# Kernel tuning notes

Hardware: AMD Instinct MI355X
Metric: run time of the kernel (lower is better)

Reference implementation:

```python
import jax, jax.numpy as jnp
import numpy as np

HEADS = 8
HEAD_DIM = 32
INNER = HEADS * HEAD_DIM  # 256
DIM = 256
WS = 8            # window_size
DISP = WS // 2    # displacement for shifted windows
SCALE = HEAD_DIM ** -0.5
NEG_INF = float('-inf')


def _rel_indices(ws):
    # [ws^2, ws^2, 2] relative (dy, dx) offsets shifted to be >= 0
    idx = np.array([[x, y] for x in range(ws) for y in range(ws)])
    return idx[None, :, :] - idx[:, None, :] + ws - 1

REL = _rel_indices(WS)


def _create_mask(ws, disp, upper_lower, left_right):
    m = np.zeros((ws * ws, ws * ws), dtype=np.float32)
    if upper_lower:
        m[-disp * ws:, :-disp * ws] = NEG_INF
        m[:-disp * ws, -disp * ws:] = NEG_INF
    if left_right:
        m = m.reshape(ws, ws, ws, ws)
        m[:, -disp:, :, :-disp] = NEG_INF
        m[:, :-disp, :, -disp:] = NEG_INF
        m = m.reshape(ws * ws, ws * ws)
    return m

UL_MASK = _create_mask(WS, DISP, True, False)
LR_MASK = _create_mask(WS, DISP, False, True)


def setup_inputs() -> dict:
    key = jax.random.key(0)
    k1, k2, k3, k4 = jax.random.split(key, 4)
    x = jax.random.normal(k1, (8, 128, 128, DIM), dtype=jnp.float32)
    w_qkv = jax.random.normal(k2, (DIM, 3 * INNER), dtype=jnp.float32) * 0.02
    pos_embedding = jax.random.normal(k3, (2 * WS - 1, 2 * WS - 1), dtype=jnp.float32)
    w_out = jax.random.normal(k4, (INNER, DIM), dtype=jnp.float32) * 0.02
    b_out = jnp.zeros((DIM,), dtype=jnp.float32)
    return {"x": x, "w_qkv": w_qkv, "pos_embedding": pos_embedding,
            "w_out": w_out, "b_out": b_out}


def reference(x, w_qkv, pos_embedding, w_out, b_out):
    b, H, W, _ = x.shape
    nwh, nww = H // WS, W // WS
    nw = nwh * nww

    # cyclic shift (shifted=True)
    xs = jnp.roll(x, (-DISP, -DISP), axis=(1, 2))

    qkv = xs @ w_qkv  # [b, H, W, 3*INNER]
    q, k, v = jnp.split(qkv, 3, axis=-1)

    def to_windows(t):
        # [b,H,W,INNER] -> [b, heads, nw, ws*ws, head_dim]
        t = t.reshape(b, nwh, WS, nww, WS, HEADS, HEAD_DIM)
        return t.transpose(0, 5, 1, 3, 2, 4, 6).reshape(b, HEADS, nw, WS * WS, HEAD_DIM)

    q, k, v = to_windows(q), to_windows(k), to_windows(v)

    dots = jnp.einsum('bhwid,bhwjd->bhwij', q, k) * SCALE

    # relative position bias gather: [ws^2, ws^2]
    bias = pos_embedding[REL[..., 0], REL[..., 1]]
    dots = dots + bias

    # shifted-window mask (static per grid): [nw, ws^2, ws^2]
    mask = np.zeros((nw, WS * WS, WS * WS), dtype=np.float32)
    mask[-nww:] += UL_MASK
    mask[nww - 1::nww] += LR_MASK
    dots = dots + jnp.asarray(mask)

    attn = jax.nn.softmax(dots, axis=-1)
    out = jnp.einsum('bhwij,bhwjd->bhwid', attn, v)

    # windows -> [b, H, W, INNER]
    out = out.reshape(b, HEADS, nwh, nww, WS, WS, HEAD_DIM)
    out = out.transpose(0, 2, 4, 3, 5, 1, 6).reshape(b, H, W, INNER)

    out = out @ w_out + b_out
    out = jnp.roll(out, (DISP, DISP), axis=(1, 2))  # cyclic back shift
    return out
```

## Files before the change

### kernel.cpp

```cpp
#include <hip/hip_runtime.h>
#include <hip/hip_bf16.h>


typedef __attribute__((ext_vector_type(8)))  short bf16x8;
typedef __attribute__((ext_vector_type(16))) float f32x16;

#define MFMA32(a, b, c) __builtin_amdgcn_mfma_f32_32x32x16_bf16((a), (b), (c), 0, 0, 0)

#define QK_SCALE 0.17677669529663687f
#define LOG2E    1.44269504088896340f

__device__ __forceinline__ uint32_t pack2(float lo, float hi) {
  float2 f2; f2.x = lo; f2.y = hi;
  __hip_bfloat162 h2 = __float22bfloat162_rn(f2);
  union { __hip_bfloat162 h; uint32_t u; } cv;
  cv.h = h2;
  return cv.u;
}

__device__ __forceinline__ bf16x8 frag_from_u4(uint32_t a, uint32_t b,
                                               uint32_t c, uint32_t d) {
  union { uint32_t u[4]; bf16x8 v; } r;
  r.u[0] = a; r.u[1] = b; r.u[2] = c; r.u[3] = d;
  return r.v;
}

__device__ __forceinline__ bf16x8 makefrag(const f32x16& a, int kt, int hf) {
  const int b0 = kt * 8;
  uint32_t q0 = pack2(a[b0 + 0], a[b0 + 1]);
  uint32_t q1 = pack2(a[b0 + 2], a[b0 + 3]);
  uint32_t q2 = pack2(a[b0 + 4], a[b0 + 5]);
  uint32_t q3 = pack2(a[b0 + 6], a[b0 + 7]);
  uint32_t x0 = (uint32_t)__shfl_xor((int)q0, 32, 64);
  uint32_t x1 = (uint32_t)__shfl_xor((int)q1, 32, 64);
  uint32_t x2 = (uint32_t)__shfl_xor((int)q2, 32, 64);
  uint32_t x3 = (uint32_t)__shfl_xor((int)q3, 32, 64);
  uint32_t d0 = hf ? x2 : q0;
  uint32_t d1 = hf ? x3 : q1;
  uint32_t d2 = hf ? q2 : x0;
  uint32_t d3 = hf ? q3 : x1;
  return frag_from_u4(d0, d1, d2, d3);
}

__global__ void prep_weights(const float* __restrict__ wqkv,
                             const float* __restrict__ wout,
                             const float* __restrict__ pos,
                             ushort* __restrict__ Wpack,
                             ushort* __restrict__ WoPack,
                             float* __restrict__ Bpack) {
  int id = blockIdx.x * 256 + threadIdx.x;
  if (id < 196608) {
    int sec = id >> 16;
    int j = id & 65535;
    int h = j >> 13, kt = (j >> 9) & 15, lane = (j >> 3) & 63, i = j & 7;
    int n = h * 32 + (lane & 31);
    int k = kt * 16 + (lane >> 5) * 8 + i;
    float v = wqkv[k * 768 + sec * 256 + n];
    if (sec == 0) v *= QK_SCALE;
    Wpack[id] = __bfloat16_as_ushort(__float2bfloat16(v));
  } else if (id < 262144) {
    int j = id - 196608;
    int h = j >> 13, kt = (j >> 9) & 15, lane = (j >> 3) & 63, i = j & 7;
    int n = h * 32 + (lane & 31);
    int k = kt * 16 + (lane >> 5) * 8 + i;
    WoPack[j] = __bfloat16_as_ushort(__float2bfloat16(wout[k * 256 + n]));
  } else if (id < 278528) {
    int j = id - 262144;
    int type = j >> 12;
    int r12 = j & 4095;
    int ai = r12 >> 11, bi = (r12 >> 10) & 1, rb = (r12 >> 8) & 3;
    int lane = (r12 >> 2) & 63, jj = r12 & 3;
    int n = jj + 8 * rb + 4 * (lane >> 5) + 32 * ai;
    int m = (lane & 31) + 32 * bi;
    float v = pos[((n >> 3) - (m >> 3) + 7) * 15 + ((n & 7) - (m & 7) + 7)];
    bool ul = (m >= 32) != (n >= 32);
    bool lr = ((m & 7) >= 4) != ((n & 7) >= 4);
    if (((type & 2) && ul) || ((type & 1) && lr)) v = -1e30f;
    Bpack[j] = v;
  }
}

__global__ __launch_bounds__(512, 2) void swin_attn(
    const float* __restrict__ x, const float* __restrict__ bout,
    const ushort* __restrict__ Wpack, const ushort* __restrict__ WoPack,
    const float* __restrict__ Bpack, float* __restrict__ out) {
  __shared__ uint4 lds[32 * 64];
  uint4*  ldsX = lds;
  ushort* ldsO = (ushort*)lds;

  const int bid = blockIdx.x;
  const int b  = bid >> 8;
  const int wy = (bid >> 4) & 15;
  const int wx = bid & 15;
  const int t    = threadIdx.x;
  const int lane = t & 63;
  const int h    = t >> 6;
  const int l31  = lane & 31;
  const int hf   = lane >> 5;

  f32x16 zf;
  #pragma unroll
  for (int i = 0; i < 16; ++i) zf[i] = 0.0f;

  {
    int tok = t >> 3, kc = t & 7;
    int ty = tok >> 3, tx = tok & 7;
    int yy = (wy * 8 + ty + 4) & 127;
    int xx = (wx * 8 + tx + 4) & 127;
    const float* xr = x + (((b * 128 + yy) * 128 + xx) << 8) + kc * 32;
    #pragma unroll
    for (int g = 0; g < 4; ++g) {
      float4 a = *(const float4*)(xr + g * 8);
      float4 c = *(const float4*)(xr + g * 8 + 4);
      uint4 w;
      w.x = pack2(a.x, a.y); w.y = pack2(a.z, a.w);
      w.z = pack2(c.x, c.y); w.w = pack2(c.z, c.w);
      int kg = kc * 4 + g;
      ldsX[(kg * 64 + tok) ^ kc] = w;
    }
  }
  __syncthreads();

  const ushort* wqp = Wpack + h * 8192;
  const ushort* wkp = wqp + 65536;
  const ushort* wvp = wkp + 65536;

  bf16x8 fQ[2][2];
  {
    f32x16 a0 = zf, a1 = zf;
    #pragma unroll 4
    for (int kt = 0; kt < 16; ++kt) {
      int kg = 2 * kt + hf;
      uint4 ux0 = ldsX[(kg * 64 + l31) ^ (kg >> 2)];
      uint4 ux1 = ldsX[(kg * 64 + 32 + l31) ^ (kg >> 2)];
      bf16x8 xf0 = frag_from_u4(ux0.x, ux0.y, ux0.z, ux0.w);
      bf16x8 xf1 = frag_from_u4(ux1.x, ux1.y, ux1.z, ux1.w);
      bf16x8 fw = *(const bf16x8*)(wqp + kt * 512 + lane * 8);
      a0 = MFMA32(fw, xf0, a0);  a1 = MFMA32(fw, xf1, a1);
    }
    #pragma unroll
    for (int kt = 0; kt < 2; ++kt) {
      fQ[0][kt] = makefrag(a0, kt, hf);
      fQ[1][kt] = makefrag(a1, kt, hf);
    }
  }

  bf16x8 fK[2][2];
  {
    f32x16 a0 = zf, a1 = zf;
    #pragma unroll 4
    for (int kt = 0; kt < 16; ++kt) {
      int kg = 2 * kt + hf;
      uint4 ux0 = ldsX[(kg * 64 + l31) ^ (kg >> 2)];
      uint4 ux1 = ldsX[(kg * 64 + 32 + l31) ^ (kg >> 2)];
      bf16x8 xf0 = frag_from_u4(ux0.x, ux0.y, ux0.z, ux0.w);
      bf16x8 xf1 = frag_from_u4(ux1.x, ux1.y, ux1.z, ux1.w);
      bf16x8 fw = *(const bf16x8*)(wkp + kt * 512 + lane * 8);
      a0 = MFMA32(fw, xf0, a0);  a1 = MFMA32(fw, xf1, a1);
    }
    #pragma unroll
    for (int kt = 0; kt < 2; ++kt) {
      fK[0][kt] = makefrag(a0, kt, hf);
      fK[1][kt] = makefrag(a1, kt, hf);
    }
  }

  const float* Bp = Bpack + ((((wy == 15) ? 2 : 0) | ((wx == 15) ? 1 : 0)) << 12);
  bf16x8 pf[2][4];
  float ri[2];
  #pragma unroll
  for (int bi = 0; bi < 2; ++bi) {
    f32x16 s0, s1;
    #pragma unroll
    for (int rb = 0; rb < 4; ++rb) {
      float4 f0 = *(const float4*)(Bp + ((bi * 4 + rb) * 64 + lane) * 4);
      float4 f1 = *(const float4*)(Bp + (((2 + bi) * 4 + rb) * 64 + lane) * 4);
      s0[rb * 4 + 0] = f0.x; s0[rb * 4 + 1] = f0.y;
      s0[rb * 4 + 2] = f0.z; s0[rb * 4 + 3] = f0.w;
      s1[rb * 4 + 0] = f1.x; s1[rb * 4 + 1] = f1.y;
      s1[rb * 4 + 2] = f1.z; s1[rb * 4 + 3] = f1.w;
    }
    #pragma unroll
    for (int kt = 0; kt < 2; ++kt) {
      s0 = MFMA32(fK[0][kt], fQ[bi][kt], s0);
      s1 = MFMA32(fK[1][kt], fQ[bi][kt], s1);
    }
    float mx = -3e38f;
    #pragma unroll
    for (int r = 0; r < 16; ++r) mx = fmaxf(mx, fmaxf(s0[r], s1[r]));
    mx = fmaxf(mx, __shfl_xor(mx, 32, 64));
    float sum = 0.0f;
    #pragma unroll
    for (int r = 0; r < 16; ++r) {
      float p0 = exp2f((s0[r] - mx) * LOG2E);
      float p1 = exp2f((s1[r] - mx) * LOG2E);
      s0[r] = p0; s1[r] = p1;
      sum += p0 + p1;
    }
    sum += __shfl_xor(sum, 32, 64);
    ri[bi] = 1.0f / sum;
    #pragma unroll
    for (int kt = 0; kt < 2; ++kt) {
      pf[bi][kt]     = makefrag(s0, kt, hf);
      pf[bi][2 + kt] = makefrag(s1, kt, hf);
    }
  }

  bf16x8 fV[2][2];
  {
    f32x16 a0 = zf, a1 = zf;
    #pragma unroll 4
    for (int kt = 0; kt < 16; ++kt) {
      int kg = 2 * kt + hf;
      uint4 ux0 = ldsX[(kg * 64 + l31) ^ (kg >> 2)];
      uint4 ux1 = ldsX[(kg * 64 + 32 + l31) ^ (kg >> 2)];
      bf16x8 xf0 = frag_from_u4(ux0.x, ux0.y, ux0.z, ux0.w);
      bf16x8 xf1 = frag_from_u4(ux1.x, ux1.y, ux1.z, ux1.w);
      bf16x8 fw = *(const bf16x8*)(wvp + kt * 512 + lane * 8);
      a0 = MFMA32(xf0, fw, a0);  a1 = MFMA32(xf1, fw, a1);
    }
    #pragma unroll
    for (int kt = 0; kt < 2; ++kt) {
      fV[0][kt] = makefrag(a0, kt, hf);
      fV[1][kt] = makefrag(a1, kt, hf);
    }
  }

  f32x16 ot[2];
  ot[0] = zf; ot[1] = zf;
  #pragma unroll
  for (int jt = 0; jt < 4; ++jt) {
    bf16x8 aV = fV[jt >> 1][jt & 1];
    ot[0] = MFMA32(aV, pf[0][jt], ot[0]);
    ot[1] = MFMA32(aV, pf[1][jt], ot[1]);
  }
  #pragma unroll
  for (int bi = 0; bi < 2; ++bi)
    #pragma unroll
    for (int r = 0; r < 16; ++r) ot[bi][r] *= ri[bi];

  __syncthreads();

  {
    #pragma unroll
    for (int bi = 0; bi < 2; ++bi) {
      int tok = bi * 32 + l31;
      #pragma unroll
      for (int g = 0; g < 4; ++g) {
        int kg = h * 4 + g;
        uint2 wv2;
        wv2.x = pack2(ot[bi][4 * g + 0], ot[bi][4 * g + 1]);
        wv2.y = pack2(ot[bi][4 * g + 2], ot[bi][4 * g + 3]);
        *(uint2*)&ldsO[(kg * 64 + tok) * 8 + 4 * hf] = wv2;
      }
    }
  }
  __syncthreads();

  const ushort* wop = WoPack + h * 8192;
  f32x16 u[2];
  u[0] = zf; u[1] = zf;
  #pragma unroll 4
  for (int kt = 0; kt < 16; ++kt) {
    int kg = 2 * kt + hf;
    bf16x8 wa = *(const bf16x8*)(wop + kt * 512 + lane * 8);
    bf16x8 b0 = *(const bf16x8*)&ldsO[(kg * 64 + l31) * 8];
    bf16x8 b1 = *(const bf16x8*)&ldsO[(kg * 64 + 32 + l31) * 8];
    u[0] = MFMA32(wa, b0, u[0]);
    u[1] = MFMA32(wa, b1, u[1]);
  }

  #pragma unroll
  for (int tt = 0; tt < 2; ++tt) {
    int tok = 32 * tt + l31;
    int ty = tok >> 3, tx = tok & 7;
    int yy = (wy * 8 + ty + 4) & 127;
    int xx = (wx * 8 + tx + 4) & 127;
    float* ob = out + (((b * 128 + yy) * 128 + xx) << 8);
    #pragma unroll
    for (int g = 0; g < 4; ++g) {
      int c0 = h * 32 + 8 * g + 4 * hf;
      float4 bo = *(const float4*)(bout + c0);
      float4 v;
      v.x = (tt ? u[1][4 * g + 0] : u[0][4 * g + 0]) + bo.x;
      v.y = (tt ? u[1][4 * g + 1] : u[0][4 * g + 1]) + bo.y;
      v.z = (tt ? u[1][4 * g + 2] : u[0][4 * g + 2]) + bo.z;
      v.w = (tt ? u[1][4 * g + 3] : u[0][4 * g + 3]) + bo.w;
      *(float4*)(ob + c0) = v;
    }
  }
}

extern "C" void kernel_launch(void* const* d_in, const int* in_sizes, int n_in,
                              void* d_out, int out_size, void* d_ws, size_t ws_size,
                              hipStream_t stream) {
  const float* x    = (const float*)d_in[0];
  const float* wqkv = (const float*)d_in[1];
  const float* pos  = (const float*)d_in[2];
  const float* wout = (const float*)d_in[3];
  const float* bout = (const float*)d_in[4];

  ushort* Wpack  = (ushort*)d_ws;
  ushort* WoPack = Wpack + 196608;
  float*  Bpack  = (float*)((char*)d_ws + 524288);

  prep_weights<<<1088, 256, 0, stream>>>(wqkv, wout, pos, Wpack, WoPack, Bpack);
  swin_attn<<<2048, 512, 0, stream>>>(x, bout, Wpack, WoPack, Bpack, (float*)d_out);
}
```

Before: 140.3 us.

## Process two adjacent windows per block to reuse weight fragments

Each block now computes two neighbouring shifted windows instead of one. Every weight fragment fetched from global memory feeds four MFMAs instead of two, and the grid is halved. This targets redundant weight loads per window. In exchange, LDS use doubles and register pressure rises, which may reduce occupancy or cause spills under the existing launch bounds.

Result: slower. 158.7 us (+13.1%).

```diff
diff --git a/kernel.cpp b/kernel.cpp
--- a/kernel.cpp
+++ b/kernel.cpp
@@ -84,14 +84,14 @@
     const float* __restrict__ x, const float* __restrict__ bout,
     const ushort* __restrict__ Wpack, const ushort* __restrict__ WoPack,
     const float* __restrict__ Bpack, float* __restrict__ out) {
-  __shared__ uint4 lds[32 * 64];
+  __shared__ uint4 lds[2 * 32 * 64];
   uint4*  ldsX = lds;
   ushort* ldsO = (ushort*)lds;
 
   const int bid = blockIdx.x;
-  const int b  = bid >> 8;
-  const int wy = (bid >> 4) & 15;
-  const int wx = bid & 15;
+  const int b   = bid >> 7;
+  const int wy  = (bid >> 3) & 15;
+  const int wxp = bid & 7;
   const int t    = threadIdx.x;
   const int lane = t & 63;
   const int h    = t >> 6;
@@ -106,17 +106,21 @@
     int tok = t >> 3, kc = t & 7;
     int ty = tok >> 3, tx = tok & 7;
     int yy = (wy * 8 + ty + 4) & 127;
-    int xx = (wx * 8 + tx + 4) & 127;
-    const float* xr = x + (((b * 128 + yy) * 128 + xx) << 8) + kc * 32;
-    #pragma unroll
-    for (int g = 0; g < 4; ++g) {
-      float4 a = *(const float4*)(xr + g * 8);
-      float4 c = *(const float4*)(xr + g * 8 + 4);
-      uint4 w;
-      w.x = pack2(a.x, a.y); w.y = pack2(a.z, a.w);
-      w.z = pack2(c.x, c.y); w.w = pack2(c.z, c.w);
-      int kg = kc * 4 + g;
-      ldsX[(kg * 64 + tok) ^ kc] = w;
+    #pragma unroll
+    for (int w = 0; w < 2; ++w) {
+      int wx = wxp * 2 + w;
+      int xx = (wx * 8 + tx + 4) & 127;
+      const float* xr = x + (((b * 128 + yy) * 128 + xx) << 8) + kc * 32;
+      #pragma unroll
+      for (int g = 0; g < 4; ++g) {
+        float4 a = *(const float4*)(xr + g * 8);
+        float4 c = *(const float4*)(xr + g * 8 + 4);
+        uint4 wv;
+        wv.x = pack2(a.x, a.y); wv.y = pack2(a.z, a.w);
+        wv.z = pack2(c.x, c.y); wv.w = pack2(c.z, c.w);
+        int kg = kc * 4 + g;
+        ldsX[w * 2048 + ((kg * 64 + tok) ^ kc)] = wv;
+      }
     }
   }
   __syncthreads();
@@ -125,123 +129,149 @@
   const ushort* wkp = wqp + 65536;
   const ushort* wvp = wkp + 65536;
 
-  bf16x8 fQ[2][2];
+  bf16x8 fQ0[2][2], fQ1[2][2];
   {
-    f32x16 a0 = zf, a1 = zf;
-    #pragma unroll 4
+    f32x16 a00 = zf, a01 = zf, a10 = zf, a11 = zf;
+    #pragma unroll 2
     for (int kt = 0; kt < 16; ++kt) {
       int kg = 2 * kt + hf;
-      uint4 ux0 = ldsX[(kg * 64 + l31) ^ (kg >> 2)];
-      uint4 ux1 = ldsX[(kg * 64 + 32 + l31) ^ (kg >> 2)];
-      bf16x8 xf0 = frag_from_u4(ux0.x, ux0.y, ux0.z, ux0.w);
-      bf16x8 xf1 = frag_from_u4(ux1.x, ux1.y, ux1.z, ux1.w);
+      int s0i = (kg * 64 + l31) ^ (kg >> 2);
+      int s1i = (kg * 64 + 32 + l31) ^ (kg >> 2);
+      uint4 u00 = ldsX[s0i],        u01 = ldsX[s1i];
+      uint4 u10 = ldsX[2048 + s0i], u11 = ldsX[2048 + s1i];
       bf16x8 fw = *(const bf16x8*)(wqp + kt * 512 + lane * 8);
-      a0 = MFMA32(fw, xf0, a0);  a1 = MFMA32(fw, xf1, a1);
+      a00 = MFMA32(fw, frag_from_u4(u00.x, u00.y, u00.z, u00.w), a00);
+      a01 = MFMA32(fw, frag_from_u4(u01.x, u01.y, u01.z, u01.w), a01);
+      a10 = MFMA32(fw, frag_from_u4(u10.x, u10.y, u10.z, u10.w), a10);
+      a11 = MFMA32(fw, frag_from_u4(u11.x, u11.y, u11.z, u11.w), a11);
     }
     #pragma unroll
     for (int kt = 0; kt < 2; ++kt) {
-      fQ[0][kt] = makefrag(a0, kt, hf);
-      fQ[1][kt] = makefrag(a1, kt, hf);
-    }
-  }
-
-  bf16x8 fK[2][2];
+      fQ0[0][kt] = makefrag(a00, kt, hf);
+      fQ0[1][kt] = makefrag(a01, kt, hf);
+      fQ1[0][kt] = makefrag(a10, kt, hf);
+      fQ1[1][kt] = makefrag(a11, kt, hf);
+    }
+  }
+
+  bf16x8 fK0[2][2], fK1[2][2];
   {
-    f32x16 a0 = zf, a1 = zf;
-    #pragma unroll 4
+    f32x16 a00 = zf, a01 = zf, a10 = zf, a11 = zf;
+    #pragma unroll 2
     for (int kt = 0; kt < 16; ++kt) {
       int kg = 2 * kt + hf;
-      uint4 ux0 = ldsX[(kg * 64 + l31) ^ (kg >> 2)];
-      uint4 ux1 = ldsX[(kg * 64 + 32 + l31) ^ (kg >> 2)];
-      bf16x8 xf0 = frag_from_u4(ux0.x, ux0.y, ux0.z, ux0.w);
-      bf16x8 xf1 = frag_from_u4(ux1.x, ux1.y, ux1.z, ux1.w);
+      int s0i = (kg * 64 + l31) ^ (kg >> 2);
+      int s1i = (kg * 64 + 32 + l31) ^ (kg >> 2);
+      uint4 u00 = ldsX[s0i],        u01 = ldsX[s1i];
+      uint4 u10 = ldsX[2048 + s0i], u11 = ldsX[2048 + s1i];
       bf16x8 fw = *(const bf16x8*)(wkp + kt * 512 + lane * 8);
-      a0 = MFMA32(fw, xf0, a0);  a1 = MFMA32(fw, xf1, a1);
+      a00 = MFMA32(fw, frag_from_u4(u00.x, u00.y, u00.z, u00.w), a00);
+      a01 = MFMA32(fw, frag_from_u4(u01.x, u01.y, u01.z, u01.w), a01);
+      a10 = MFMA32(fw, frag_from_u4(u10.x, u10.y, u10.z, u10.w), a10);
+      a11 = MFMA32(fw, frag_from_u4(u11.x, u11.y, u11.z, u11.w), a11);
     }
     #pragma unroll
     for (int kt = 0; kt < 2; ++kt) {
-      fK[0][kt] = makefrag(a0, kt, hf);
-      fK[1][kt] = makefrag(a1, kt, hf);
-    }
-  }
-
-  const float* Bp = Bpack + ((((wy == 15) ? 2 : 0) | ((wx == 15) ? 1 : 0)) << 12);
-  bf16x8 pf[2][4];
-  float ri[2];
+      fK0[0][kt] = makefrag(a00, kt, hf);
+      fK0[1][kt] = makefrag(a01, kt, hf);
+      fK1[0][kt] = makefrag(a10, kt, hf);
+      fK1[1][kt] = makefrag(a11, kt, hf);
+    }
+  }
+
+  bf16x8 pf0[2][4], pf1[2][4];
+  float ri0[2], ri1[2];
+  const int tybase = (wy == 15) ? 2 : 0;
   #pragma unroll
-  for (int bi = 0; bi < 2; ++bi) {
-    f32x16 s0, s1;
-    #pragma unroll
-    for (int rb = 0; rb < 4; ++rb) {
-      float4 f0 = *(const float4*)(Bp + ((bi * 4 + rb) * 64 + lane) * 4);
-      float4 f1 = *(const float4*)(Bp + (((2 + bi) * 4 + rb) * 64 + lane) * 4);
-      s0[rb * 4 + 0] = f0.x; s0[rb * 4 + 1] = f0.y;
-      s0[rb * 4 + 2] = f0.z; s0[rb * 4 + 3] = f0.w;
-      s1[rb * 4 + 0] = f1.x; s1[rb * 4 + 1] = f1.y;
-      s1[rb * 4 + 2] = f1.z; s1[rb * 4 + 3] = f1.w;
-    }
-    #pragma unroll
-    for (int kt = 0; kt < 2; ++kt) {
-      s0 = MFMA32(fK[0][kt], fQ[bi][kt], s0);
-      s1 = MFMA32(fK[1][kt], fQ[bi][kt], s1);
-    }
-    float mx = -3e38f;
-    #pragma unroll
-    for (int r = 0; r < 16; ++r) mx = fmaxf(mx, fmaxf(s0[r], s1[r]));
-    mx = fmaxf(mx, __shfl_xor(mx, 32, 64));
-    float sum = 0.0f;
-    #pragma unroll
-    for (int r = 0; r < 16; ++r) {
-      float p0 = exp2f((s0[r] - mx) * LOG2E);
-      float p1 = exp2f((s1[r] - mx) * LOG2E);
-      s0[r] = p0; s1[r] = p1;
-      sum += p0 + p1;
-    }
-    sum += __shfl_xor(sum, 32, 64);
-    ri[bi] = 1.0f / sum;
-    #pragma unroll
-    for (int kt = 0; kt < 2; ++kt) {
-      pf[bi][kt]     = makefrag(s0, kt, hf);
-      pf[bi][2 + kt] = makefrag(s1, kt, hf);
-    }
-  }
-
-  bf16x8 fV[2][2];
-  {
-    f32x16 a0 = zf, a1 = zf;
-    #pragma unroll 4
-    for (int kt = 0; kt < 16; ++kt) {
-      int kg = 2 * kt + hf;
-      uint4 ux0 = ldsX[(kg * 64 + l31) ^ (kg >> 2)];
-      uint4 ux1 = ldsX[(kg * 64 + 32 + l31) ^ (kg >> 2)];
-      bf16x8 xf0 = frag_from_u4(ux0.x, ux0.y, ux0.z, ux0.w);
-      bf16x8 xf1 = frag_from_u4(ux1.x, ux1.y, ux1.z, ux1.w);
-      bf16x8 fw = *(const bf16x8*)(wvp + kt * 512 + lane * 8);
-      a0 = MFMA32(xf0, fw, a0);  a1 = MFMA32(xf1, fw, a1);
-    }
-    #pragma unroll
-    for (int kt = 0; kt < 2; ++kt) {
-      fV[0][kt] = makefrag(a0, kt, hf);
-      fV[1][kt] = makefrag(a1, kt, hf);
-    }
-  }
-
-  f32x16 ot[2];
-  ot[0] = zf; ot[1] = zf;
+  for (int w = 0; w < 2; ++w) {
+    int wx = wxp * 2 + w;
+    const float* Bp = Bpack + ((tybase | ((wx == 15) ? 1 : 0)) << 12);
+    #pragma unroll
+    for (int bi = 0; bi < 2; ++bi) {
+      f32x16 s0, s1;
+      #pragma unroll
+      for (int rb = 0; rb < 4; ++rb) {
+        float4 f0 = *(const float4*)(Bp + ((bi * 4 + rb) * 64 + lane) * 4);
+        float4 f1 = *(const float4*)(Bp + (((2 + bi) * 4 + rb) * 64 + lane) * 4);
+        s0[rb * 4 + 0] = f0.x; s0[rb * 4 + 1] = f0.y;
+        s0[rb * 4 + 2] = f0.z; s0[rb * 4 + 3] = f0.w;
+        s1[rb * 4 + 0] = f1.x; s1[rb * 4 + 1] = f1.y;
+        s1[rb * 4 + 2] = f1.z; s1[rb * 4 + 3] = f1.w;
+      }
+      #pragma unroll
+      for (int kt = 0; kt < 2; ++kt) {
+        s0 = MFMA32(w ? fK1[0][kt] : fK0[0][kt],
+                    w ? fQ1[bi][kt] : fQ0[bi][kt], s0);
+        s1 = MFMA32(w ? fK1[1][kt] : fK0[1][kt],
+                    w ? fQ1[bi][kt] : fQ0[bi][kt], s1);
+      }
+      float mx = -3e38f;
+      #pragma unroll
+      for (int r = 0; r < 16; ++r) mx = fmaxf(mx, fmaxf(s0[r], s1[r]));
+      mx = fmaxf(mx, __shfl_xor(mx, 32, 64));
+      float sum = 0.0f;
+      #pragma unroll
+      for (int r = 0; r < 16; ++r) {
+        float p0 = exp2f((s0[r] - mx) * LOG2E);
+        float p1 = exp2f((s1[r] - mx) * LOG2E);
+        s0[r] = p0; s1[r] = p1;
+        sum += p0 + p1;
+      }
+      sum += __shfl_xor(sum, 32, 64);
+      float rv = 1.0f / sum;
+      if (w) ri1[bi] = rv; else ri0[bi] = rv;
+      #pragma unroll
+      for (int kt = 0; kt < 2; ++kt) {
+        if (w) {
+          pf1[bi][kt]     = makefrag(s0, kt, hf);
+          pf1[bi][2 + kt] = makefrag(s1, kt, hf);
+        } else {
+          pf0[bi][kt]     = makefrag(s0, kt, hf);
+          pf0[bi][2 + kt] = makefrag(s1, kt, hf);
+        }
+      }
+    }
+  }
+
   #pragma unroll
-  for (int jt = 0; jt < 4; ++jt) {
-    bf16x8 aV = fV[jt >> 1][jt & 1];
-    ot[0] = MFMA32(aV, pf[0][jt], ot[0]);
-    ot[1] = MFMA32(aV, pf[1][jt], ot[1]);
-  }
-  #pragma unroll
-  for (int bi = 0; bi < 2; ++bi)
-    #pragma unroll
-    for (int r = 0; r < 16; ++r) ot[bi][r] *= ri[bi];
-
-  __syncthreads();
-
-  {
+  for (int w = 0; w < 2; ++w) {
+    bf16x8 fV[2][2];
+    {
+      f32x16 a0 = zf, a1 = zf;
+      #pragma unroll 2
+      for (int kt = 0; kt < 16; ++kt) {
+        int kg = 2 * kt + hf;
+        int s0i = (kg * 64 + l31) ^ (kg >> 2);
+        int s1i = (kg * 64 + 32 + l31) ^ (kg >> 2);
+        uint4 ux0 = ldsX[w * 2048 + s0i];
+        uint4 ux1 = ldsX[w * 2048 + s1i];
+        bf16x8 fw = *(const bf16x8*)(wvp + kt * 512 + lane * 8);
+        a0 = MFMA32(frag_from_u4(ux0.x, ux0.y, ux0.z, ux0.w), fw, a0);
+        a1 = MFMA32(frag_from_u4(ux1.x, ux1.y, ux1.z, ux1.w), fw, a1);
+      }
+      #pragma unroll
+      for (int kt = 0; kt < 2; ++kt) {
+        fV[0][kt] = makefrag(a0, kt, hf);
+        fV[1][kt] = makefrag(a1, kt, hf);
+      }
+    }
+    __syncthreads();
+
+    f32x16 ot[2];
+    ot[0] = zf; ot[1] = zf;
+    #pragma unroll
+    for (int jt = 0; jt < 4; ++jt) {
+      bf16x8 aV = fV[jt >> 1][jt & 1];
+      ot[0] = MFMA32(aV, w ? pf1[0][jt] : pf0[0][jt], ot[0]);
+      ot[1] = MFMA32(aV, w ? pf1[1][jt] : pf0[1][jt], ot[1]);
+    }
+    #pragma unroll
+    for (int bi = 0; bi < 2; ++bi) {
+      float rv = w ? ri1[bi] : ri0[bi];
+      #pragma unroll
+      for (int r = 0; r < 16; ++r) ot[bi][r] *= rv;
+    }
+
     #pragma unroll
     for (int bi = 0; bi < 2; ++bi) {
       int tok = bi * 32 + l31;
@@ -251,42 +281,48 @@
         uint2 wv2;
         wv2.x = pack2(ot[bi][4 * g + 0], ot[bi][4 * g + 1]);
         wv2.y = pack2(ot[bi][4 * g + 2], ot[bi][4 * g + 3]);
-        *(uint2*)&ldsO[(kg * 64 + tok) * 8 + 4 * hf] = wv2;
+        *(uint2*)&ldsO[w * 16384 + (kg * 64 + tok) * 8 + 4 * hf] = wv2;
       }
     }
   }
   __syncthreads();
 
   const ushort* wop = WoPack + h * 8192;
-  f32x16 u[2];
-  u[0] = zf; u[1] = zf;
-  #pragma unroll 4
+  f32x16 u00 = zf, u01 = zf, u10 = zf, u11 = zf;
+  #pragma unroll 2
   for (int kt = 0; kt < 16; ++kt) {
     int kg = 2 * kt + hf;
     bf16x8 wa = *(const bf16x8*)(wop + kt * 512 + lane * 8);
-    bf16x8 b0 = *(const bf16x8*)&ldsO[(kg * 64 + l31) * 8];
-    bf16x8 b1 = *(const bf16x8*)&ldsO[(kg * 64 + 32 + l31) * 8];
-    u[0] = MFMA32(wa, b0, u[0]);
-    u[1] = MFMA32(wa, b1, u[1]);
+    bf16x8 b00 = *(const bf16x8*)&ldsO[(kg * 64 + l31) * 8];
+    bf16x8 b01 = *(const bf16x8*)&ldsO[(kg * 64 + 32 + l31) * 8];
+    bf16x8 b10 = *(const bf16x8*)&ldsO[16384 + (kg * 64 + l31) * 8];
+    bf16x8 b11 = *(const bf16x8*)&ldsO[16384 + (kg * 64 + 32 + l31) * 8];
+    u00 = MFMA32(wa, b00, u00);  u01 = MFMA32(wa, b01, u01);
+    u10 = MFMA32(wa, b10, u10);  u11 = MFMA32(wa, b11, u11);
   }
 
   #pragma unroll
-  for (int tt = 0; tt < 2; ++tt) {
-    int tok = 32 * tt + l31;
-    int ty = tok >> 3, tx = tok & 7;
-    int yy = (wy * 8 + ty + 4) & 127;
-    int xx = (wx * 8 + tx + 4) & 127;
-    float* ob = out + (((b * 128 + yy) * 128 + xx) << 8);
-    #pragma unroll
-    for (int g = 0; g < 4; ++g) {
-      int c0 = h * 32 + 8 * g + 4 * hf;
-      float4 bo = *(const float4*)(bout + c0);
-      float4 v;
-      v.x = (tt ? u[1][4 * g + 0] : u[0][4 * g + 0]) + bo.x;
-      v.y = (tt ? u[1][4 * g + 1] : u[0][4 * g + 1]) + bo.y;
-      v.z = (tt ? u[1][4 * g + 2] : u[0][4 * g + 2]) + bo.z;
-      v.w = (tt ? u[1][4 * g + 3] : u[0][4 * g + 3]) + bo.w;
-      *(float4*)(ob + c0) = v;
+  for (int w = 0; w < 2; ++w) {
+    int wx = wxp * 2 + w;
+    #pragma unroll
+    for (int tt = 0; tt < 2; ++tt) {
+      const f32x16& u = w ? (tt ? u11 : u10) : (tt ? u01 : u00);
+      int tok = 32 * tt + l31;
+      int ty = tok >> 3, tx = tok & 7;
+      int yy = (wy * 8 + ty + 4) & 127;
+      int xx = (wx * 8 + tx + 4) & 127;
+      float* ob = out + (((b * 128 + yy) * 128 + xx) << 8);
+      #pragma unroll
+      for (int g = 0; g < 4; ++g) {
+        int c0 = h * 32 + 8 * g + 4 * hf;
+        float4 bo = *(const float4*)(bout + c0);
+        float4 v;
+        v.x = u[4 * g + 0] + bo.x;
+        v.y = u[4 * g + 1] + bo.y;
+        v.z = u[4 * g + 2] + bo.z;
+        v.w = u[4 * g + 3] + bo.w;
+        *(float4*)(ob + c0) = v;
+      }
     }
   }
 }
@@ -305,5 +341,5 @@
   float*  Bpack  = (float*)((char*)d_ws + 524288);
 
   prep_weights<<<1088, 256, 0, stream>>>(wqkv, wout, pos, Wpack, WoPack, Bpack);
-  swin_attn<<<2048, 512, 0, stream>>>(x, bout, Wpack, WoPack, Bpack, (float*)d_out);
-}
+  swin_attn<<<1024, 512, 0, stream>>>(x, bout, Wpack, WoPack, Bpack, (float*)d_out);
+}
```
